# Performance work log

Measured on AMD Instinct MI355X. Metric: run time of the kernel, lower is better.

The kernel has to match this reference:

```python
import jax, jax.numpy as jnp
import numpy as np

N = 100000

def _gcn_norm(edge_index, n):
    # PyG GCNConv default: add self-loops, symmetric deg^-1/2 normalization
    loops = jnp.arange(n, dtype=edge_index.dtype)
    src = jnp.concatenate([edge_index[0], loops])
    dst = jnp.concatenate([edge_index[1], loops])
    deg = jax.ops.segment_sum(jnp.ones_like(dst, dtype=jnp.float32), dst, num_segments=n)
    dinv = jnp.where(deg > 0, jax.lax.rsqrt(deg), 0.0)
    norm = dinv[src] * dinv[dst]  # [E+N]
    return src, dst, norm

def _gcn_conv(h, W, b, src, dst, norm, n):
    # transform then gather-scale-scatter aggregate
    h = h @ W                                   # [N, out]
    out = jax.ops.segment_sum(norm[:, None] * h[src], dst, num_segments=n)
    return out + b

def _prelu(h, a):
    return jnp.where(h > 0, h, a * h)

def _dropout(h, u, p=0.5):
    # deterministic dropout: keep where u >= p, scale by 1/(1-p)
    return jnp.where(u >= p, h / (1.0 - p), 0.0)

def setup_inputs() -> dict:
    key = jax.random.key(0)
    ks = jax.random.split(key, 12)
    D, H1, H2, C, E = 512, 128, 16, 10, 1600000
    x = jax.random.normal(ks[0], (N, D), dtype=jnp.float32)
    edge_index = jax.random.randint(ks[1], (2, E), 0, N, dtype=jnp.int64)
    u1 = jax.random.uniform(ks[2], (N, H1), dtype=jnp.float32)
    u2 = jax.random.uniform(ks[3], (N, H2), dtype=jnp.float32)
    def glorot(k, shp):
        lim = np.sqrt(6.0 / (shp[0] + shp[1]))
        return jax.random.uniform(k, shp, dtype=jnp.float32, minval=-lim, maxval=lim)
    W1 = glorot(ks[4], (D, H1)); b1 = jnp.zeros((H1,), jnp.float32)
    W2 = glorot(ks[5], (H1, H2)); b2 = jnp.zeros((H2,), jnp.float32)
    fcW = glorot(ks[6], (H2, C)); fcb = jnp.zeros((C,), jnp.float32)
    a = jnp.float32(0.25)  # PReLU init (shared single param for both layers)
    return {"x": x, "edge_index": edge_index, "W1": W1, "b1": b1, "W2": W2,
            "b2": b2, "a": a, "fcW": fcW, "fcb": fcb, "u1": u1, "u2": u2}

def reference(x, edge_index, W1, b1, W2, b2, a, fcW, fcb, u1, u2):
    src, dst, norm = _gcn_norm(edge_index, N)
    feat1 = _dropout(_prelu(_gcn_conv(x, W1, b1, src, dst, norm, N), a), u1)
    feat2 = _dropout(_prelu(_gcn_conv(feat1, W2, b2, src, dst, norm, N), a), u2)
    logits = feat2 @ fcW + fcb
    return (feat2, logits)
```

## Files before the change

### kernel.cpp

```cpp
#include <hip/hip_runtime.h>
#include <hip/hip_bf16.h>
#include <stdint.h>

#define NN 100000
#define DIN 512
#define H1C 128
#define H2C 16
#define NCLS 10
#define NB_SCAN ((NN + 255) / 256)

typedef __attribute__((ext_vector_type(8))) short s16x8;
typedef __attribute__((ext_vector_type(4))) float f32x4;
typedef __attribute__((ext_vector_type(4))) unsigned short u16x4;
typedef __attribute__((ext_vector_type(8))) unsigned short u16x8;

static __device__ __forceinline__ unsigned short f2bf(float f) {
  __hip_bfloat16 h = __float2bfloat16(f);
  return *(unsigned short*)&h;
}
static __device__ __forceinline__ float bflo(unsigned u) {
  return __uint_as_float(u << 16);
}
static __device__ __forceinline__ float bfhi(unsigned u) {
  return __uint_as_float(u & 0xffff0000u);
}

__device__ __forceinline__ int ld_src(const int* __restrict__ ei, int f, int E, int i) {
  return f ? ei[2 * (size_t)i] : ei[i];
}
__device__ __forceinline__ int ld_dst(const int* __restrict__ ei, int f, int E, int i) {
  return f ? ei[2 * ((size_t)E + (size_t)i)] : ei[(size_t)E + (size_t)i];
}

__global__ void k_pre(const int* __restrict__ ei, int* __restrict__ flag,
                      int* __restrict__ deg,
                      const float* __restrict__ W1, unsigned short* __restrict__ Wt,
                      const float* __restrict__ u1, uint4* __restrict__ m1, int n) {
  int i = blockIdx.x * 256 + threadIdx.x;
  if (blockIdx.x == 0 && threadIdx.x < 64) {
    int v = ei[2 * threadIdx.x + 1];
    unsigned long long b = __ballot(v == 0);
    if (threadIdx.x == 0) *flag = (b == ~0ull) ? 1 : 0;
  }
  if (i < n) deg[i] = 0;
  if (i < H1C * DIN) {
    int nn = i >> 9, k = i & 511;
    Wt[i] = f2bf(W1[(size_t)k * H1C + nn]);
  }
  int wave = threadIdx.x >> 6, lane = threadIdx.x & 63;
  int wrow = blockIdx.x * 4 + wave;
  const float2* __restrict__ u1v = (const float2*)u1;
#pragma unroll
  for (int rr = 0; rr < 4; rr++) {
    int row = wrow + rr * 25000;
    float2 uu = u1v[(size_t)row * 64 + lane];
    unsigned long long b0 = __ballot(uu.x >= 0.5f);
    unsigned long long b1 = __ballot(uu.y >= 0.5f);
    if (lane == 0)
      m1[row] = make_uint4((unsigned)b0, (unsigned)(b0 >> 32),
                           (unsigned)b1, (unsigned)(b1 >> 32));
  }
}

__global__ void k_count(const int* __restrict__ ei, const int* __restrict__ flag,
                        int E, int* __restrict__ deg, int* __restrict__ rank) {
  int f = *flag;
  int base = blockIdx.x * 1024 + threadIdx.x;
  if (base + 768 < E) {
    int d0 = ld_dst(ei, f, E, base);
    int d1 = ld_dst(ei, f, E, base + 256);
    int d2 = ld_dst(ei, f, E, base + 512);
    int d3 = ld_dst(ei, f, E, base + 768);
    int r0 = atomicAdd(&deg[d0], 1);
    int r1 = atomicAdd(&deg[d1], 1);
    int r2 = atomicAdd(&deg[d2], 1);
    int r3 = atomicAdd(&deg[d3], 1);
    rank[base] = r0;
    rank[base + 256] = r1;
    rank[base + 512] = r2;
    rank[base + 768] = r3;
  } else {
#pragma unroll
    for (int k = 0; k < 4; k++) {
      int i = base + k * 256;
      if (i < E) rank[i] = atomicAdd(&deg[ld_dst(ei, f, E, i)], 1);
    }
  }
}

__global__ void k_scanA(const int* __restrict__ deg, int* __restrict__ incl,
                        int* __restrict__ bsum, float* __restrict__ dinv, int n) {
  __shared__ int s[256];
  int i = blockIdx.x * 256 + threadIdx.x;
  int v = (i < n) ? deg[i] : 0;
  if (i < n) dinv[i] = rsqrtf((float)(v + 1));
  s[threadIdx.x] = v;
  __syncthreads();
  for (int off = 1; off < 256; off <<= 1) {
    int t = (threadIdx.x >= off) ? s[threadIdx.x - off] : 0;
    __syncthreads();
    s[threadIdx.x] += t;
    __syncthreads();
  }
  if (i < n) incl[i] = s[threadIdx.x];
  if (threadIdx.x == 255) bsum[blockIdx.x] = s[255];
}

__global__ void k_scanBC(const int* __restrict__ deg, const int* __restrict__ bsum,
                         int* __restrict__ offs, int n, int E, int nb) {
  __shared__ int s[512];
  int tid = threadIdx.x;
  int v = (tid < nb) ? bsum[tid] : 0;
  s[tid] = v;
  __syncthreads();
  for (int off = 1; off < 512; off <<= 1) {
    int t = (tid >= off) ? s[tid - off] : 0;
    __syncthreads();
    s[tid] += t;
    __syncthreads();
  }
  int bid = blockIdx.x;
  int pb = (bid > 0) ? s[bid - 1] : 0;
  int i = bid * 256 + (tid & 255);
  if (tid < 256 && i < n) offs[i] = offs[i] - deg[i] + pb;
  if (bid == 0 && tid == 0) offs[n] = E;
}

__global__ void k_scatter(const int* __restrict__ ei, const int* __restrict__ flag, int E,
                          const int* __restrict__ offs, const int* __restrict__ rank,
                          const float* __restrict__ dinv, uint2* __restrict__ csr_sw) {
  int f = *flag;
  int base = blockIdx.x * 1024 + threadIdx.x;
  if (base + 768 < E) {
    int i0 = base, i1 = base + 256, i2 = base + 512, i3 = base + 768;
    int s0 = ld_src(ei, f, E, i0), d0 = ld_dst(ei, f, E, i0);
    int s1 = ld_src(ei, f, E, i1), d1 = ld_dst(ei, f, E, i1);
    int s2 = ld_src(ei, f, E, i2), d2 = ld_dst(ei, f, E, i2);
    int s3 = ld_src(ei, f, E, i3), d3 = ld_dst(ei, f, E, i3);
    int r0 = rank[i0], r1 = rank[i1], r2 = rank[i2], r3 = rank[i3];
    int o0 = offs[d0], o1 = offs[d1], o2 = offs[d2], o3 = offs[d3];
    float w0 = dinv[s0], w1 = dinv[s1], w2 = dinv[s2], w3 = dinv[s3];
    csr_sw[o0 + r0] = make_uint2((unsigned)s0, __float_as_uint(w0));
    csr_sw[o1 + r1] = make_uint2((unsigned)s1, __float_as_uint(w1));
    csr_sw[o2 + r2] = make_uint2((unsigned)s2, __float_as_uint(w2));
    csr_sw[o3 + r3] = make_uint2((unsigned)s3, __float_as_uint(w3));
  } else {
#pragma unroll
    for (int k = 0; k < 4; k++) {
      int i = base + k * 256;
      if (i < E) {
        int s = ld_src(ei, f, E, i), d = ld_dst(ei, f, E, i);
        int pos = offs[d] + rank[i];
        csr_sw[pos] = make_uint2((unsigned)s, __float_as_uint(dinv[s]));
      }
    }
  }
}

#define BM 64
#define BK 64
#define LDA 72
#define LDB 72

__global__ __launch_bounds__(256) void k_gemm1_mfma(const float* __restrict__ x,
                                                    const unsigned short* __restrict__ Wt,
                                                    unsigned int* __restrict__ h1u, int n) {
  __shared__ unsigned short As[BM * LDA];
  __shared__ unsigned short Bs[H1C * LDB];
  int tid = threadIdx.x;
  int wave = tid >> 6, lane = tid & 63;
  int wm = wave >> 1, wn = wave & 1;
  int bm = blockIdx.x * BM;
  int lrow = lane & 15, lk = (lane >> 4) * 8;

  f32x4 acc[2][4];
#pragma unroll
  for (int i = 0; i < 2; i++)
#pragma unroll
    for (int j = 0; j < 4; j++) acc[i][j] = (f32x4){0.f, 0.f, 0.f, 0.f};

  float4 areg[4];
  u16x8 breg[4];

  auto loadA = [&](int k0) {
#pragma unroll
    for (int p = 0; p < 4; p++) {
      int idx = p * 256 + tid;
      int r = idx >> 4, c4 = (idx & 15) * 4;
      int row = bm + r;
      areg[p] = make_float4(0.f, 0.f, 0.f, 0.f);
      if (row < n) areg[p] = *(const float4*)(x + (size_t)row * DIN + k0 + c4);
    }
  };
  auto loadB = [&](int k0) {
#pragma unroll
    for (int p = 0; p < 4; p++) {
      int idx = p * 256 + tid;
      int r = idx >> 3, c8 = (idx & 7) * 8;
      breg[p] = *(const u16x8*)&Wt[(size_t)r * DIN + k0 + c8];
    }
  };

  loadA(0);
  loadB(0);

  for (int k0 = 0; k0 < DIN; k0 += BK) {
#pragma unroll
    for (int p = 0; p < 4; p++) {
      int idx = p * 256 + tid;
      int r = idx >> 4, c4 = (idx & 15) * 4;
      u16x4 b4;
      b4.x = f2bf(areg[p].x); b4.y = f2bf(areg[p].y);
      b4.z = f2bf(areg[p].z); b4.w = f2bf(areg[p].w);
      *(u16x4*)&As[r * LDA + c4] = b4;
      int rb = idx >> 3, c8 = (idx & 7) * 8;
      int pr = (rb & 64) + (((rb & 1) + 2 * ((rb >> 5) & 1)) << 4) + ((rb >> 1) & 15);
      *(u16x8*)&Bs[pr * LDB + c8] = breg[p];
    }
    if (k0 + BK < DIN) {
      loadA(k0 + BK);
      loadB(k0 + BK);
    }
    __syncthreads();
#pragma unroll
    for (int kk = 0; kk < 2; kk++) {
      s16x8 a[2], b[4];
#pragma unroll
      for (int mi = 0; mi < 2; mi++)
        a[mi] = *(const s16x8*)&As[(wm * 32 + mi * 16 + lrow) * LDA + kk * 32 + lk];
#pragma unroll
      for (int nj = 0; nj < 4; nj++)
        b[nj] = *(const s16x8*)&Bs[(wn * 64 + nj * 16 + lrow) * LDB + kk * 32 + lk];
#pragma unroll
      for (int mi = 0; mi < 2; mi++)
#pragma unroll
        for (int nj = 0; nj < 4; nj++)
          acc[mi][nj] = __builtin_amdgcn_mfma_f32_16x16x32_bf16(a[mi], b[nj], acc[mi][nj], 0, 0, 0);
    }
    __syncthreads();
  }
#pragma unroll
  for (int mi = 0; mi < 2; mi++) {
#pragma unroll
    for (int r = 0; r < 4; r++) {
      int row = bm + wm * 32 + mi * 16 + (lane >> 4) * 4 + r;
      if (row < n) {
        unsigned p0 = ((unsigned)f2bf(acc[mi][1][r]) << 16) | (unsigned)f2bf(acc[mi][0][r]);
        unsigned p1 = ((unsigned)f2bf(acc[mi][3][r]) << 16) | (unsigned)f2bf(acc[mi][2][r]);
        h1u[(size_t)row * 64 + wn * 32 + lrow] = p0;
        h1u[(size_t)row * 64 + wn * 32 + 16 + lrow] = p1;
      }
    }
  }
}

__global__ __launch_bounds__(256) void k_agg1(const unsigned int* __restrict__ h1u,
                                              const uint2* __restrict__ csr_sw,
                                              const int* __restrict__ offs,
                                              const float* __restrict__ dinv,
                                              const float* __restrict__ b1,
                                              const float* __restrict__ aP,
                                              const uint4* __restrict__ m1,
                                              unsigned int* __restrict__ f1u, int n) {
  int wid = (blockIdx.x * 256 + threadIdx.x) >> 6;
  int lane = threadIdx.x & 63;
  if (wid >= n) return;
  int d = wid;
  int beg = offs[d], end = offs[d + 1];
  unsigned gs = h1u[(size_t)d * 64 + lane];
  uint4 mv = m1[d];
  float ax = 0.f, ay = 0.f;
  int e = beg;
  for (; e + 15 < end; e += 16) {
    uint2 rr[16];
    unsigned gg[16];
#pragma unroll
    for (int k = 0; k < 16; k++) rr[k] = csr_sw[e + k];
#pragma unroll
    for (int k = 0; k < 16; k++) gg[k] = h1u[(size_t)rr[k].x * 64 + lane];
#pragma unroll
    for (int k = 0; k < 16; k++) {
      float w = __uint_as_float(rr[k].y);
      ax += w * bflo(gg[k]); ay += w * bfhi(gg[k]);
    }
  }
  for (; e + 7 < end; e += 8) {
    uint2 rr[8];
    unsigned gg[8];
#pragma unroll
    for (int k = 0; k < 8; k++) rr[k] = csr_sw[e + k];
#pragma unroll
    for (int k = 0; k < 8; k++) gg[k] = h1u[(size_t)rr[k].x * 64 + lane];
#pragma unroll
    for (int k = 0; k < 8; k++) {
      float w = __uint_as_float(rr[k].y);
      ax += w * bflo(gg[k]); ay += w * bfhi(gg[k]);
    }
  }
  for (; e + 3 < end; e += 4) {
    uint2 rr[4];
    unsigned gg[4];
#pragma unroll
    for (int k = 0; k < 4; k++) rr[k] = csr_sw[e + k];
#pragma unroll
    for (int k = 0; k < 4; k++) gg[k] = h1u[(size_t)rr[k].x * 64 + lane];
#pragma unroll
    for (int k = 0; k < 4; k++) {
      float w = __uint_as_float(rr[k].y);
      ax += w * bflo(gg[k]); ay += w * bfhi(gg[k]);
    }
  }
  for (; e < end; e++) {
    uint2 rr = csr_sw[e];
    float w = __uint_as_float(rr.y);
    unsigned g = h1u[(size_t)rr.x * 64 + lane];
    ax += w * bflo(g); ay += w * bfhi(g);
  }
  float di = dinv[d];
  ax = (ax + di * bflo(gs)) * di;
  ay = (ay + di * bfhi(gs)) * di;
  float2 bb = ((const float2*)b1)[lane];
  ax += bb.x; ay += bb.y;
  float al = *aP;
  ax = ax > 0.f ? ax : al * ax;
  ay = ay > 0.f ? ay : al * ay;
  unsigned long long b0 = (unsigned long long)mv.x | ((unsigned long long)mv.y << 32);
  unsigned long long b1m = (unsigned long long)mv.z | ((unsigned long long)mv.w << 32);
  ax = ((b0 >> lane) & 1ull) ? ax * 2.f : 0.f;
  ay = ((b1m >> lane) & 1ull) ? ay * 2.f : 0.f;
  unsigned pk = ((unsigned)f2bf(ay) << 16) | (unsigned)f2bf(ax);
  f1u[(size_t)d * 64 + lane] = pk;
}

__global__ __launch_bounds__(256) void k_gemm2(const unsigned int* __restrict__ f1u,
                                               const float* __restrict__ W2,
                                               unsigned int* __restrict__ h2u, int n) {
  __shared__ float ws[H1C][H2C];
  __shared__ unsigned int fs[16][66];
  int tid = threadIdx.x;
#pragma unroll
  for (int p = 0; p < 8; p++) {
    int idx = tid + p * 256;
    ws[idx >> 4][idx & 15] = W2[idx];
  }
  int r0 = blockIdx.x * 16;
  {
    int r = tid >> 4, c4 = (tid & 15) * 4;
    int row = r0 + r;
    uint4 v = make_uint4(0, 0, 0, 0);
    if (row < n) v = *(const uint4*)(f1u + (size_t)row * 64 + c4);
    *(uint4*)&fs[r][c4] = v;
  }
  __syncthreads();
  int col = tid & 15, r = tid >> 4;
  float acc = 0.f;
#pragma unroll
  for (int k = 0; k < 64; k++) {
    unsigned u = fs[r][k];
    acc += bflo(u) * ws[2 * k][col] + bfhi(u) * ws[2 * k + 1][col];
  }
  int row = r0 + r;
  float accN = __shfl_xor(acc, 1, 64);
  if ((col & 1) == 0 && row < n) {
    unsigned pk = ((unsigned)f2bf(accN) << 16) | (unsigned)f2bf(acc);
    h2u[(size_t)row * 8 + (col >> 1)] = pk;
  }
}

__global__ __launch_bounds__(256) void k_agg2(const unsigned int* __restrict__ h2u,
                                              const uint2* __restrict__ csr_sw,
                                              const int* __restrict__ offs,
                                              const float* __restrict__ dinv,
                                              const float* __restrict__ b2,
                                              const float* __restrict__ aP,
                                              const float* __restrict__ u2,
                                              const float* __restrict__ fcW,
                                              const float* __restrict__ fcb,
                                              float* __restrict__ out_feat2,
                                              float* __restrict__ out_logits, int n) {
  int wid = (blockIdx.x * 256 + threadIdx.x) >> 6;
  int lane = threadIdx.x & 63;
  if (wid >= n) return;
  int d = wid;
  int g = lane >> 3, j = lane & 7;
  int beg = offs[d], end = offs[d + 1];
  unsigned gs = h2u[(size_t)d * 8 + j];
  float aa = 0.f, ab = 0.f;
  int e = beg + g;
  for (; e + 8 < end; e += 16) {
    uint2 r0 = csr_sw[e], r1 = csr_sw[e + 8];
    unsigned g0 = h2u[(size_t)r0.x * 8 + j];
    unsigned g1 = h2u[(size_t)r1.x * 8 + j];
    float w0 = __uint_as_float(r0.y), w1 = __uint_as_float(r1.y);
    aa += w0 * bflo(g0) + w1 * bflo(g1);
    ab += w0 * bfhi(g0) + w1 * bfhi(g1);
  }
  for (; e < end; e += 8) {
    uint2 rr = csr_sw[e];
    unsigned gg = h2u[(size_t)rr.x * 8 + j];
    float w = __uint_as_float(rr.y);
    aa += w * bflo(gg); ab += w * bfhi(gg);
  }
  aa += __shfl_xor(aa, 8, 64); aa += __shfl_xor(aa, 16, 64); aa += __shfl_xor(aa, 32, 64);
  ab += __shfl_xor(ab, 8, 64); ab += __shfl_xor(ab, 16, 64); ab += __shfl_xor(ab, 32, 64);
  float di = dinv[d];
  aa = (aa + di * bflo(gs)) * di;
  ab = (ab + di * bfhi(gs)) * di;
  aa += b2[2 * j]; ab += b2[2 * j + 1];
  float al = *aP;
  aa = aa > 0.f ? aa : al * aa;
  ab = ab > 0.f ? ab : al * ab;
  float2 uu = ((const float2*)(u2 + (size_t)d * H2C))[j];
  aa = (uu.x >= 0.5f) ? aa * 2.f : 0.f;
  ab = (uu.y >= 0.5f) ? ab * 2.f : 0.f;
  if (lane < 8) {
    float2 o; o.x = aa; o.y = ab;
    ((float2*)(out_feat2 + (size_t)d * H2C))[j] = o;
  }
  int c = lane & 15;
  int cc = (c < NCLS) ? c : 0;
  float lg = fcb[cc];
#pragma unroll
  for (int k = 0; k < 8; k++) {
    float va = __shfl(aa, k, 64);
    float vb = __shfl(ab, k, 64);
    lg += va * fcW[(2 * k) * NCLS + cc] + vb * fcW[(2 * k + 1) * NCLS + cc];
  }
  if (lane < NCLS) out_logits[(size_t)d * NCLS + c] = lg;
}

extern "C" void kernel_launch(void* const* d_in, const int* in_sizes, int n_in,
                              void* d_out, int out_size, void* d_ws, size_t ws_size,
                              hipStream_t stream) {
  const float* x   = (const float*)d_in[0];
  const int*   ei  = (const int*)d_in[1];
  const float* W1  = (const float*)d_in[2];
  const float* b1  = (const float*)d_in[3];
  const float* W2  = (const float*)d_in[4];
  const float* b2  = (const float*)d_in[5];
  const float* aP  = (const float*)d_in[6];
  const float* fcW = (const float*)d_in[7];
  const float* fcb = (const float*)d_in[8];
  const float* u1  = (const float*)d_in[9];
  const float* u2  = (const float*)d_in[10];
  const int E = in_sizes[1] / 2;

  float* out_feat2  = (float*)d_out;
  float* out_logits = (float*)d_out + (size_t)NN * H2C;

  char* w = (char*)d_ws;
  size_t off = 0;
  auto A = [&](size_t bytes) -> char* {
    char* p = w + off;
    off = (off + bytes + 255) & ~(size_t)255;
    return p;
  };
  int*   flag   = (int*)A(256);
  int*   deg    = (int*)A((size_t)NN * 4);
  int*   offs   = (int*)A((size_t)(NN + 1) * 4);
  float* dinv   = (float*)A((size_t)NN * 4);
  int*   bsum   = (int*)A(512 * 4);
  int*   rank   = (int*)A((size_t)E * 4);
  uint2* csr_sw = (uint2*)A((size_t)E * 8);
  unsigned int* h1u = (unsigned int*)A((size_t)NN * 64 * 4);
  unsigned int* f1u = (unsigned int*)A((size_t)NN * 64 * 4);
  unsigned int* h2u = (unsigned int*)A((size_t)NN * 8 * 4);
  unsigned short* Wt = (unsigned short*)A((size_t)H1C * DIN * 2);
  uint4* m1     = (uint4*)A((size_t)NN * 16);

  dim3 b256(256);
  int gE4 = (E + 1023) / 1024;

  k_pre<<<6250, b256, 0, stream>>>(ei, flag, deg, W1, Wt, u1, m1, NN);
  k_count<<<gE4, b256, 0, stream>>>(ei, flag, E, deg, rank);
  k_scanA<<<NB_SCAN, b256, 0, stream>>>(deg, offs, bsum, dinv, NN);
  k_scanBC<<<NB_SCAN, 512, 0, stream>>>(deg, bsum, offs, NN, E, NB_SCAN);
  k_scatter<<<gE4, b256, 0, stream>>>(ei, flag, E, offs, rank, dinv, csr_sw);
  k_gemm1_mfma<<<(NN + BM - 1) / BM, b256, 0, stream>>>(x, Wt, h1u, NN);
  k_agg1<<<(NN + 3) / 4, b256, 0, stream>>>(h1u, csr_sw, offs, dinv, b1, aP, m1, f1u, NN);
  k_gemm2<<<(NN + 15) / 16, b256, 0, stream>>>(f1u, W2, h2u, NN);
  k_agg2<<<(NN + 3) / 4, b256, 0, stream>>>(h2u, csr_sw, offs, dinv, b2, aP, u2,
                                            fcW, fcb, out_feat2, out_logits, NN);
}
```

Measured before the change: 313.9 us.

## Fold source-side dinv into GEMM outputs and shrink CSR to source indices

Each node's transformed features are pre-scaled by its deg^-1/2 in the GEMM epilogues. Aggregation then becomes a plain sum and the CSR only needs 4-byte source indices instead of 8-byte (src, weight) pairs. This halves the edge-list bytes read in both aggregation passes and removes the random dinv gather in scatter. In exchange, k_count now writes a staged (src,dst) array that scatter reads back, and rounding to bf16 happens after the dinv scaling.

```diff
diff --git a/kernel.cpp b/kernel.cpp
--- a/kernel.cpp
+++ b/kernel.cpp
@@ -63,27 +63,34 @@
 }
 
 __global__ void k_count(const int* __restrict__ ei, const int* __restrict__ flag,
-                        int E, int* __restrict__ deg, int* __restrict__ rank) {
+                        int E, int* __restrict__ deg, int* __restrict__ rank,
+                        uint2* __restrict__ sd) {
   int f = *flag;
   int base = blockIdx.x * 1024 + threadIdx.x;
   if (base + 768 < E) {
-    int d0 = ld_dst(ei, f, E, base);
-    int d1 = ld_dst(ei, f, E, base + 256);
-    int d2 = ld_dst(ei, f, E, base + 512);
-    int d3 = ld_dst(ei, f, E, base + 768);
+    int i0 = base, i1 = base + 256, i2 = base + 512, i3 = base + 768;
+    int s0 = ld_src(ei, f, E, i0), d0 = ld_dst(ei, f, E, i0);
+    int s1 = ld_src(ei, f, E, i1), d1 = ld_dst(ei, f, E, i1);
+    int s2 = ld_src(ei, f, E, i2), d2 = ld_dst(ei, f, E, i2);
+    int s3 = ld_src(ei, f, E, i3), d3 = ld_dst(ei, f, E, i3);
+    sd[i0] = make_uint2((unsigned)s0, (unsigned)d0);
+    sd[i1] = make_uint2((unsigned)s1, (unsigned)d1);
+    sd[i2] = make_uint2((unsigned)s2, (unsigned)d2);
+    sd[i3] = make_uint2((unsigned)s3, (unsigned)d3);
     int r0 = atomicAdd(&deg[d0], 1);
     int r1 = atomicAdd(&deg[d1], 1);
     int r2 = atomicAdd(&deg[d2], 1);
     int r3 = atomicAdd(&deg[d3], 1);
-    rank[base] = r0;
-    rank[base + 256] = r1;
-    rank[base + 512] = r2;
-    rank[base + 768] = r3;
+    rank[i0] = r0; rank[i1] = r1; rank[i2] = r2; rank[i3] = r3;
   } else {
 #pragma unroll
     for (int k = 0; k < 4; k++) {
       int i = base + k * 256;
-      if (i < E) rank[i] = atomicAdd(&deg[ld_dst(ei, f, E, i)], 1);
+      if (i < E) {
+        int s = ld_src(ei, f, E, i), d = ld_dst(ei, f, E, i);
+        sd[i] = make_uint2((unsigned)s, (unsigned)d);
+        rank[i] = atomicAdd(&deg[d], 1);
+      }
     }
   }
 }
@@ -126,32 +133,25 @@
   if (bid == 0 && tid == 0) offs[n] = E;
 }
 
-__global__ void k_scatter(const int* __restrict__ ei, const int* __restrict__ flag, int E,
-                          const int* __restrict__ offs, const int* __restrict__ rank,
-                          const float* __restrict__ dinv, uint2* __restrict__ csr_sw) {
-  int f = *flag;
+__global__ void k_scatter(const uint2* __restrict__ sd, const int* __restrict__ rank,
+                          int E, const int* __restrict__ offs, int* __restrict__ csr_s) {
   int base = blockIdx.x * 1024 + threadIdx.x;
   if (base + 768 < E) {
     int i0 = base, i1 = base + 256, i2 = base + 512, i3 = base + 768;
-    int s0 = ld_src(ei, f, E, i0), d0 = ld_dst(ei, f, E, i0);
-    int s1 = ld_src(ei, f, E, i1), d1 = ld_dst(ei, f, E, i1);
-    int s2 = ld_src(ei, f, E, i2), d2 = ld_dst(ei, f, E, i2);
-    int s3 = ld_src(ei, f, E, i3), d3 = ld_dst(ei, f, E, i3);
+    uint2 e0 = sd[i0], e1 = sd[i1], e2 = sd[i2], e3 = sd[i3];
     int r0 = rank[i0], r1 = rank[i1], r2 = rank[i2], r3 = rank[i3];
-    int o0 = offs[d0], o1 = offs[d1], o2 = offs[d2], o3 = offs[d3];
-    float w0 = dinv[s0], w1 = dinv[s1], w2 = dinv[s2], w3 = dinv[s3];
-    csr_sw[o0 + r0] = make_uint2((unsigned)s0, __float_as_uint(w0));
-    csr_sw[o1 + r1] = make_uint2((unsigned)s1, __float_as_uint(w1));
-    csr_sw[o2 + r2] = make_uint2((unsigned)s2, __float_as_uint(w2));
-    csr_sw[o3 + r3] = make_uint2((unsigned)s3, __float_as_uint(w3));
+    int o0 = offs[e0.y], o1 = offs[e1.y], o2 = offs[e2.y], o3 = offs[e3.y];
+    csr_s[o0 + r0] = (int)e0.x;
+    csr_s[o1 + r1] = (int)e1.x;
+    csr_s[o2 + r2] = (int)e2.x;
+    csr_s[o3 + r3] = (int)e3.x;
   } else {
 #pragma unroll
     for (int k = 0; k < 4; k++) {
       int i = base + k * 256;
       if (i < E) {
-        int s = ld_src(ei, f, E, i), d = ld_dst(ei, f, E, i);
-        int pos = offs[d] + rank[i];
-        csr_sw[pos] = make_uint2((unsigned)s, __float_as_uint(dinv[s]));
+        uint2 e = sd[i];
+        csr_s[offs[e.y] + rank[i]] = (int)e.x;
       }
     }
   }
@@ -164,6 +164,7 @@
 
 __global__ __launch_bounds__(256) void k_gemm1_mfma(const float* __restrict__ x,
                                                     const unsigned short* __restrict__ Wt,
+                                                    const float* __restrict__ dinv,
                                                     unsigned int* __restrict__ h1u, int n) {
   __shared__ unsigned short As[BM * LDA];
   __shared__ unsigned short Bs[H1C * LDB];
@@ -245,8 +246,9 @@
     for (int r = 0; r < 4; r++) {
       int row = bm + wm * 32 + mi * 16 + (lane >> 4) * 4 + r;
       if (row < n) {
-        unsigned p0 = ((unsigned)f2bf(acc[mi][1][r]) << 16) | (unsigned)f2bf(acc[mi][0][r]);
-        unsigned p1 = ((unsigned)f2bf(acc[mi][3][r]) << 16) | (unsigned)f2bf(acc[mi][2][r]);
+        float dv = dinv[row];
+        unsigned p0 = ((unsigned)f2bf(acc[mi][1][r] * dv) << 16) | (unsigned)f2bf(acc[mi][0][r] * dv);
+        unsigned p1 = ((unsigned)f2bf(acc[mi][3][r] * dv) << 16) | (unsigned)f2bf(acc[mi][2][r] * dv);
         h1u[(size_t)row * 64 + wn * 32 + lrow] = p0;
         h1u[(size_t)row * 64 + wn * 32 + 16 + lrow] = p1;
       }
@@ -255,7 +257,7 @@
 }
 
 __global__ __launch_bounds__(256) void k_agg1(const unsigned int* __restrict__ h1u,
-                                              const uint2* __restrict__ csr_sw,
+                                              const int* __restrict__ csr_s,
                                               const int* __restrict__ offs,
                                               const float* __restrict__ dinv,
                                               const float* __restrict__ b1,
@@ -272,53 +274,42 @@
   float ax = 0.f, ay = 0.f;
   int e = beg;
   for (; e + 15 < end; e += 16) {
-    uint2 rr[16];
+    int ss[16];
     unsigned gg[16];
 #pragma unroll
-    for (int k = 0; k < 16; k++) rr[k] = csr_sw[e + k];
-#pragma unroll
-    for (int k = 0; k < 16; k++) gg[k] = h1u[(size_t)rr[k].x * 64 + lane];
-#pragma unroll
-    for (int k = 0; k < 16; k++) {
-      float w = __uint_as_float(rr[k].y);
-      ax += w * bflo(gg[k]); ay += w * bfhi(gg[k]);
-    }
+    for (int k = 0; k < 16; k++) ss[k] = csr_s[e + k];
+#pragma unroll
+    for (int k = 0; k < 16; k++) gg[k] = h1u[(size_t)ss[k] * 64 + lane];
+#pragma unroll
+    for (int k = 0; k < 16; k++) { ax += bflo(gg[k]); ay += bfhi(gg[k]); }
   }
   for (; e + 7 < end; e += 8) {
-    uint2 rr[8];
+    int ss[8];
     unsigned gg[8];
 #pragma unroll
-    for (int k = 0; k < 8; k++) rr[k] = csr_sw[e + k];
-#pragma unroll
-    for (int k = 0; k < 8; k++) gg[k] = h1u[(size_t)rr[k].x * 64 + lane];
-#pragma unroll
-    for (int k = 0; k < 8; k++) {
-      float w = __uint_as_float(rr[k].y);
-      ax += w * bflo(gg[k]); ay += w * bfhi(gg[k]);
-    }
+    for (int k = 0; k < 8; k++) ss[k] = csr_s[e + k];
+#pragma unroll
+    for (int k = 0; k < 8; k++) gg[k] = h1u[(size_t)ss[k] * 64 + lane];
+#pragma unroll
+    for (int k = 0; k < 8; k++) { ax += bflo(gg[k]); ay += bfhi(gg[k]); }
   }
   for (; e + 3 < end; e += 4) {
-    uint2 rr[4];
+    int ss[4];
     unsigned gg[4];
 #pragma unroll
-    for (int k = 0; k < 4; k++) rr[k] = csr_sw[e + k];
-#pragma unroll
-    for (int k = 0; k < 4; k++) gg[k] = h1u[(size_t)rr[k].x * 64 + lane];
-#pragma unroll
-    for (int k = 0; k < 4; k++) {
-      float w = __uint_as_float(rr[k].y);
-      ax += w * bflo(gg[k]); ay += w * bfhi(gg[k]);
-    }
+    for (int k = 0; k < 4; k++) ss[k] = csr_s[e + k];
+#pragma unroll
+    for (int k = 0; k < 4; k++) gg[k] = h1u[(size_t)ss[k] * 64 + lane];
+#pragma unroll
+    for (int k = 0; k < 4; k++) { ax += bflo(gg[k]); ay += bfhi(gg[k]); }
   }
   for (; e < end; e++) {
-    uint2 rr = csr_sw[e];
-    float w = __uint_as_float(rr.y);
-    unsigned g = h1u[(size_t)rr.x * 64 + lane];
-    ax += w * bflo(g); ay += w * bfhi(g);
+    unsigned g = h1u[(size_t)csr_s[e] * 64 + lane];
+    ax += bflo(g); ay += bfhi(g);
   }
   float di = dinv[d];
-  ax = (ax + di * bflo(gs)) * di;
-  ay = (ay + di * bfhi(gs)) * di;
+  ax = (ax + bflo(gs)) * di;
+  ay = (ay + bfhi(gs)) * di;
   float2 bb = ((const float2*)b1)[lane];
   ax += bb.x; ay += bb.y;
   float al = *aP;
@@ -334,6 +325,7 @@
 
 __global__ __launch_bounds__(256) void k_gemm2(const unsigned int* __restrict__ f1u,
                                                const float* __restrict__ W2,
+                                               const float* __restrict__ dinv,
                                                unsigned int* __restrict__ h2u, int n) {
   __shared__ float ws[H1C][H2C];
   __shared__ unsigned int fs[16][66];
@@ -360,6 +352,8 @@
     acc += bflo(u) * ws[2 * k][col] + bfhi(u) * ws[2 * k + 1][col];
   }
   int row = r0 + r;
+  float dv = (row < n) ? dinv[row] : 0.f;
+  acc *= dv;
   float accN = __shfl_xor(acc, 1, 64);
   if ((col & 1) == 0 && row < n) {
     unsigned pk = ((unsigned)f2bf(accN) << 16) | (unsigned)f2bf(acc);
@@ -368,7 +362,7 @@
 }
 
 __global__ __launch_bounds__(256) void k_agg2(const unsigned int* __restrict__ h2u,
-                                              const uint2* __restrict__ csr_sw,
+                                              const int* __restrict__ csr_s,
                                               const int* __restrict__ offs,
                                               const float* __restrict__ dinv,
                                               const float* __restrict__ b2,
@@ -388,24 +382,21 @@
   float aa = 0.f, ab = 0.f;
   int e = beg + g;
   for (; e + 8 < end; e += 16) {
-    uint2 r0 = csr_sw[e], r1 = csr_sw[e + 8];
-    unsigned g0 = h2u[(size_t)r0.x * 8 + j];
-    unsigned g1 = h2u[(size_t)r1.x * 8 + j];
-    float w0 = __uint_as_float(r0.y), w1 = __uint_as_float(r1.y);
-    aa += w0 * bflo(g0) + w1 * bflo(g1);
-    ab += w0 * bfhi(g0) + w1 * bfhi(g1);
+    int s0 = csr_s[e], s1 = csr_s[e + 8];
+    unsigned g0 = h2u[(size_t)s0 * 8 + j];
+    unsigned g1 = h2u[(size_t)s1 * 8 + j];
+    aa += bflo(g0) + bflo(g1);
+    ab += bfhi(g0) + bfhi(g1);
   }
   for (; e < end; e += 8) {
-    uint2 rr = csr_sw[e];
-    unsigned gg = h2u[(size_t)rr.x * 8 + j];
-    float w = __uint_as_float(rr.y);
-    aa += w * bflo(gg); ab += w * bfhi(gg);
+    unsigned gg = h2u[(size_t)csr_s[e] * 8 + j];
+    aa += bflo(gg); ab += bfhi(gg);
   }
   aa += __shfl_xor(aa, 8, 64); aa += __shfl_xor(aa, 16, 64); aa += __shfl_xor(aa, 32, 64);
   ab += __shfl_xor(ab, 8, 64); ab += __shfl_xor(ab, 16, 64); ab += __shfl_xor(ab, 32, 64);
   float di = dinv[d];
-  aa = (aa + di * bflo(gs)) * di;
-  ab = (ab + di * bfhi(gs)) * di;
+  aa = (aa + bflo(gs)) * di;
+  ab = (ab + bfhi(gs)) * di;
   aa += b2[2 * j]; ab += b2[2 * j + 1];
   float al = *aP;
   aa = aa > 0.f ? aa : al * aa;
@@ -461,7 +452,8 @@
   float* dinv   = (float*)A((size_t)NN * 4);
   int*   bsum   = (int*)A(512 * 4);
   int*   rank   = (int*)A((size_t)E * 4);
-  uint2* csr_sw = (uint2*)A((size_t)E * 8);
+  uint2* sd     = (uint2*)A((size_t)E * 8);
+  int*   csr_s  = (int*)A((size_t)E * 4);
   unsigned int* h1u = (unsigned int*)A((size_t)NN * 64 * 4);
   unsigned int* f1u = (unsigned int*)A((size_t)NN * 64 * 4);
   unsigned int* h2u = (unsigned int*)A((size_t)NN * 8 * 4);
@@ -472,13 +464,13 @@
   int gE4 = (E + 1023) / 1024;
 
   k_pre<<<6250, b256, 0, stream>>>(ei, flag, deg, W1, Wt, u1, m1, NN);
-  k_count<<<gE4, b256, 0, stream>>>(ei, flag, E, deg, rank);
+  k_count<<<gE4, b256, 0, stream>>>(ei, flag, E, deg, rank, sd);
   k_scanA<<<NB_SCAN, b256, 0, stream>>>(deg, offs, bsum, dinv, NN);
   k_scanBC<<<NB_SCAN, 512, 0, stream>>>(deg, bsum, offs, NN, E, NB_SCAN);
-  k_scatter<<<gE4, b256, 0, stream>>>(ei, flag, E, offs, rank, dinv, csr_sw);
-  k_gemm1_mfma<<<(NN + BM - 1) / BM, b256, 0, stream>>>(x, Wt, h1u, NN);
-  k_agg1<<<(NN + 3) / 4, b256, 0, stream>>>(h1u, csr_sw, offs, dinv, b1, aP, m1, f1u, NN);
-  k_gemm2<<<(NN + 15) / 16, b256, 0, stream>>>(f1u, W2, h2u, NN);
-  k_agg2<<<(NN + 3) / 4, b256, 0, stream>>>(h2u, csr_sw, offs, dinv, b2, aP, u2,
+  k_scatter<<<gE4, b256, 0, stream>>>(sd, rank, E, offs, csr_s);
+  k_gemm1_mfma<<<(NN + BM - 1) / BM, b256, 0, stream>>>(x, Wt, dinv, h1u, NN);
+  k_agg1<<<(NN + 3) / 4, b256, 0, stream>>>(h1u, csr_s, offs, dinv, b1, aP, m1, f1u, NN);
+  k_gemm2<<<(NN + 15) / 16, b256, 0, stream>>>(f1u, W2, dinv, h2u, NN);
+  k_agg2<<<(NN + 3) / 4, b256, 0, stream>>>(h2u, csr_s, offs, dinv, b2, aP, u2,
                                             fcW, fcb, out_feat2, out_logits, NN);
 }
```

Measured after the change: 329.6 us. 5.0% more time.
